# Optimization experiments

Measured on AMD Instinct MI355X. Metric: run time of the kernel, lower is better.

The kernel has to match this reference:

```python
import jax, jax.numpy as jnp
import numpy as np

B, T, S, O, D = 1024, 512, 8, 4, 64  # batch, seq_len, sensory_dim, output_dim, hidden d (d=64 from target_params=78980)


def _w(key, shape):
    # random weights scaled ~1/sqrt(fan_in); stored as [in, out] so y = x @ W + b
    return jax.random.normal(key, shape, dtype=jnp.float32) / np.sqrt(shape[0]).astype(np.float32)


def setup_inputs() -> dict:
    key = jax.random.key(0)
    ks = jax.random.split(key, 16)
    z = lambda n: jnp.zeros((n,), jnp.float32)
    return {
        "x": jax.random.normal(ks[0], (B, T, S), dtype=jnp.float32),
        "W_enc_w": _w(ks[1], (S, D)), "W_enc_b": z(D),
        "W_from_W": _w(ks[2], (D, D)), "W_from_I": _w(ks[3], (D, D)), "W_from_A": _w(ks[4], (D, D)),
        "W_gate_w": _w(ks[5], (2 * D, D)), "W_gate_b": z(D),
        "I_z_w": _w(ks[6], (3 * D, D)), "I_z_b": z(D),
        "I_r_w": _w(ks[7], (3 * D, D)), "I_r_b": z(D),
        "I_h_w": _w(ks[8], (3 * D, D)), "I_h_b": z(D),
        "A_from_W": _w(ks[9], (D, D)), "A_from_I": _w(ks[10], (D, D)), "A_from_A": _w(ks[11], (D, D)),
        "A_gate_w": _w(ks[12], (2 * D, D)), "A_gate_b": z(D),
        "phi_w": _w(ks[13], (D, O)), "phi_b": z(O),
    }


def reference(x, W_enc_w, W_enc_b, W_from_W, W_from_I, W_from_A, W_gate_w, W_gate_b,
              I_z_w, I_z_b, I_r_w, I_r_b, I_h_w, I_h_b,
              A_from_W, A_from_I, A_from_A, A_gate_w, A_gate_b, phi_w, phi_b):
    batch = x.shape[0]
    d = W_from_W.shape[0]

    def step(carry, x_t):
        W, I, A = carry  # each [B, d]
        xt = jnp.tanh(x_t @ W_enc_w + W_enc_b)
        W_in = xt + W @ W_from_W + I @ W_from_I + A @ W_from_A
        Wg = jax.nn.sigmoid(jnp.concatenate([I, A], -1) @ W_gate_w + W_gate_b)
        W_new = jnp.tanh(W_in) * Wg
        comb = jnp.concatenate([W_new, I, A], -1)  # [B, 3d]
        z = jax.nn.sigmoid(comb @ I_z_w + I_z_b)
        r = jax.nn.sigmoid(comb @ I_r_w + I_r_b)
        h = jnp.tanh(jnp.concatenate([W_new, r * I, A], -1) @ I_h_w + I_h_b)
        I_new = (1.0 - z) * I + z * h
        A_in = W_new @ A_from_W + I_new @ A_from_I + A @ A_from_A
        Ag = jax.nn.sigmoid(jnp.concatenate([W_new, I_new], -1) @ A_gate_w + A_gate_b)
        A_new = jnp.tanh(A_in) * Ag
        action = A_new @ phi_w + phi_b  # [B, O]
        return (W_new, I_new, A_new), action

    init = tuple(jnp.zeros((batch, d), x.dtype) for _ in range(3))
    _, actions = jax.lax.scan(step, init, jnp.swapaxes(x, 0, 1))  # [T, B, O]
    return jnp.swapaxes(actions, 0, 1)  # [B, T, O]
```

## Files before the change

### kernel.cpp

```cpp
#include <hip/hip_runtime.h>
#include <cstddef>
#include <cstdint>

#define T_LEN 512
#define O_DIM 4

typedef _Float16 f16x8 __attribute__((ext_vector_type(8)));
typedef float    f32x4 __attribute__((ext_vector_type(4)));

#define MFMA(a, b, c) __builtin_amdgcn_mfma_f32_16x16x32_f16((a), (b), (c), 0, 0, 0)

__device__ __forceinline__ float sigm_f(float x) {
    return __builtin_amdgcn_rcpf(1.0f + __builtin_amdgcn_exp2f(x * -1.44269504f));
}
__device__ __forceinline__ float tanh_f(float x) {
    float e = __builtin_amdgcn_exp2f(x * 2.88539008f);
    return __builtin_fmaf(-2.0f, __builtin_amdgcn_rcpf(e + 1.0f), 1.0f);
}

__device__ __forceinline__ f16x8 load_bt(const float* __restrict__ W, int k0, int n) {
    const int lane = threadIdx.x & 63;
    const float* p = W + (size_t)(k0 + ((lane >> 4) << 3)) * 64 + n;
    f16x8 r;
#pragma unroll
    for (int j = 0; j < 8; ++j) r[j] = (_Float16)p[(size_t)j * 64];
    return r;
}

__device__ __forceinline__ f16x8 ld_af(const _Float16* base, int kt) {
    const int lane = threadIdx.x & 63;
    const int m = lane & 15, q = lane >> 4;
    return *(const f16x8*)(base + m * 72 + kt * 32 + q * 8);
}

__global__ __launch_bounds__(256, 1) void ANIMAZeroExact_86887188398421_kernel(
    const float* __restrict__ x,
    const float* __restrict__ Wenc_w, const float* __restrict__ Wenc_b,
    const float* __restrict__ WfW, const float* __restrict__ WfI, const float* __restrict__ WfA,
    const float* __restrict__ Wg_w, const float* __restrict__ Wg_b,
    const float* __restrict__ Iz_w, const float* __restrict__ Iz_b,
    const float* __restrict__ Ir_w, const float* __restrict__ Ir_b,
    const float* __restrict__ Ih_w, const float* __restrict__ Ih_b,
    const float* __restrict__ AfW, const float* __restrict__ AfI, const float* __restrict__ AfA,
    const float* __restrict__ Ag_w, const float* __restrict__ Ag_b,
    const float* __restrict__ phi_w, const float* __restrict__ phi_b,
    float* __restrict__ out)
{
    __shared__ __align__(16) _Float16 Wl[16][72];
    __shared__ __align__(16) _Float16 Il[16][72];
    __shared__ __align__(16) _Float16 Al[16][72];
    __shared__ __align__(16) _Float16 Rl[16][72];
    __shared__ __align__(16) _Float16 Ahist[16][4][72];
    __shared__ __align__(16) float xbig[4][520];
    __shared__ __align__(16) float actb[4][64][4];

    const int tid  = threadIdx.x;
    const int w    = tid >> 6;
    const int lane = tid & 63;
    const int q    = lane >> 4;
    const int c    = lane & 15;
    const int n    = w * 16 + c;
    const int r0   = blockIdx.x * 4;

    for (int i = tid; i < 16 * 72; i += 256) {
        (&Wl[0][0])[i] = (_Float16)0.0f; (&Il[0][0])[i] = (_Float16)0.0f;
        (&Al[0][0])[i] = (_Float16)0.0f; (&Rl[0][0])[i] = (_Float16)0.0f;
    }

    f16x8 S1B[6], G1B[4], ZB[6], RB[6], HB[6], AB[6], AGB[4], phiB[2];
#pragma unroll
    for (int j = 0; j < 2; ++j) {
        S1B[j] = load_bt(WfW, 32 * j, n);  S1B[2 + j] = load_bt(WfI, 32 * j, n);  S1B[4 + j] = load_bt(WfA, 32 * j, n);
        AB[j]  = load_bt(AfW, 32 * j, n);  AB[2 + j]  = load_bt(AfI, 32 * j, n);  AB[4 + j]  = load_bt(AfA, 32 * j, n);
    }
#pragma unroll
    for (int j = 0; j < 4; ++j) { G1B[j] = load_bt(Wg_w, 32 * j, n); AGB[j] = load_bt(Ag_w, 32 * j, n); }
#pragma unroll
    for (int j = 0; j < 6; ++j) { ZB[j] = load_bt(Iz_w, 32 * j, n); RB[j] = load_bt(Ir_w, 32 * j, n); HB[j] = load_bt(Ih_w, 32 * j, n); }
#pragma unroll
    for (int kt = 0; kt < 2; ++kt)
#pragma unroll
        for (int j = 0; j < 8; ++j) {
            int k = kt * 32 + q * 8 + j;
            phiB[kt][j] = (c < O_DIM) ? (_Float16)phi_w[k * O_DIM + c] : (_Float16)0.0f;
        }

    float We[8];
#pragma unroll
    for (int j = 0; j < 8; ++j) We[j] = Wenc_w[j * 64 + n];

    const float bias_g  = Wg_b[n],  bias_z = Iz_b[n], bias_r = Ir_b[n];
    const float bias_h  = Ih_b[n],  bias_ag = Ag_b[n], bias_e = Wenc_b[n];
    const float bias_p  = (c < O_DIM) ? phi_b[c] : 0.0f;

    f32x4 zero4 = {0.f, 0.f, 0.f, 0.f};

    {
        const int prow = tid >> 6, psu = tid & 63;
        const float* xg = x + (size_t)(r0 + prow) * (T_LEN * 8) + (1 + psu) * 8;
        float4 pa = *(const float4*)(xg);
        float4 pb = *(const float4*)(xg + 4);
        float* d = &xbig[prow][psu * 8];
        *(float4*)d = pa; *(float4*)(d + 4) = pb;
    }
    float xt;
    {
        const float* xg = x + (size_t)(r0 + q) * (T_LEN * 8);
        float4 a = *(const float4*)(xg);
        float4 b = *(const float4*)(xg + 4);
        float d = bias_e;
        d = __builtin_fmaf(a.x, We[0], d); d = __builtin_fmaf(a.y, We[1], d);
        d = __builtin_fmaf(a.z, We[2], d); d = __builtin_fmaf(a.w, We[3], d);
        d = __builtin_fmaf(b.x, We[4], d); d = __builtin_fmaf(b.y, We[5], d);
        d = __builtin_fmaf(b.z, We[6], d); d = __builtin_fmaf(b.w, We[7], d);
        xt = tanh_f(d);
    }

    f32x4 w_a = zero4, w_b = zero4, g_a = zero4, g_b = zero4;
    f32x4 zp_a = zero4, zp_c = zero4, rp_a = zero4, rp_c = zero4;
    f32x4 hp_a, hp_c, ap_a, ap_c, ag_a, ag_c;
    float Iv = 0.f;
    f16x8 nW0, nW1;

    __syncthreads();

#pragma unroll 1
    for (int t = 0; t < T_LEN; ++t) {
        const bool fl16 = ((t & 15) == 0) && (t > 0);
        const bool fl64 = ((t & 63) == 0) && (t > 0);

        f16x8 sA0 = ld_af(&Al[0][0], 0), sA1 = ld_af(&Al[0][0], 1);
        float4 xra = {0,0,0,0}, xrb = {0,0,0,0};
        if (fl64) {
            const int rrow = tid >> 6, rsu = tid & 63;
            int off = (t + 1 + rsu) * 8;
            if (off > T_LEN * 8 - 8) off = T_LEN * 8 - 8;
            const float* xg = x + (size_t)(r0 + rrow) * (T_LEN * 8) + off;
            xra = *(const float4*)(xg); xrb = *(const float4*)(xg + 4);
        }
        w_a = MFMA(sA0, S1B[4], w_a);  w_b = MFMA(sA1, S1B[5], w_b);
        g_a = MFMA(sA0, G1B[2], g_a);  g_b = MFMA(sA1, G1B[3], g_b);
        {
            float wn = tanh_f(xt + w_a[0] + w_b[0]) * sigm_f(g_a[0] + g_b[0] + bias_g);
            Wl[4 * q][n] = (_Float16)wn;
        }
        zp_a = MFMA(sA0, ZB[4], zp_a);  zp_c = MFMA(sA1, ZB[5], zp_c);
        rp_a = MFMA(sA0, RB[4], rp_a);  rp_c = MFMA(sA1, RB[5], rp_c);
        __syncthreads();

        nW0 = ld_af(&Wl[0][0], 0); nW1 = ld_af(&Wl[0][0], 1);
        hp_a = MFMA(sA0, HB[4], zero4); hp_c = MFMA(sA1, HB[5], zero4);
        ap_a = MFMA(sA0, AB[4], zero4); ap_c = MFMA(sA1, AB[5], zero4);
        if (fl16) {
            const _Float16* ah = &Ahist[0][0][0];
            const int hw = (4 * w + (c >> 2)) * 288 + (c & 3) * 72 + 8 * q;
            f16x8 a0 = *(const f16x8*)(ah + hw);
            f16x8 a1 = *(const f16x8*)(ah + hw + 32);
            f32x4 act = MFMA(a0, phiB[0], zero4);
            act = MFMA(a1, phiB[1], act);
            if (c < O_DIM) {
                const int slot = (t - 16 + 4 * w + q) & 63;
#pragma unroll
                for (int rg = 0; rg < 4; ++rg)
                    actb[rg][slot][c] = act[rg] + bias_p;
            }
        }
        rp_a = MFMA(nW0, RB[0], rp_a);  rp_c = MFMA(nW1, RB[1], rp_c);
        {
            float rv = sigm_f(rp_a[0] + rp_c[0] + bias_r);
            Rl[4 * q][n] = (_Float16)(rv * Iv);
        }
        zp_a = MFMA(nW0, ZB[0], zp_a);  zp_c = MFMA(nW1, ZB[1], zp_c);
        hp_a = MFMA(nW0, HB[0], hp_a);  hp_c = MFMA(nW1, HB[1], hp_c);
        w_a  = MFMA(nW0, S1B[0], zero4); w_b = MFMA(nW1, S1B[1], zero4);
        if (fl64) {
            const int rrow = tid >> 6, rsu = tid & 63;
            float* d = &xbig[rrow][rsu * 8];
            *(float4*)d = xra; *(float4*)(d + 4) = xrb;
        }
        __syncthreads();

        f16x8 hR0 = ld_af(&Rl[0][0], 0), hR1 = ld_af(&Rl[0][0], 1);
        const float* xs = &xbig[q][(t & 63) * 8];
        float4 qa = *(const float4*)xs;
        float4 qb = *(const float4*)(xs + 4);
        ap_a = MFMA(nW0, AB[0], ap_a);  ap_c = MFMA(nW1, AB[1], ap_c);
        float zv = sigm_f(zp_a[0] + zp_c[0] + bias_z);
        float xtn;
        {
            float d = bias_e;
            d = __builtin_fmaf(qa.x, We[0], d); d = __builtin_fmaf(qa.y, We[1], d);
            d = __builtin_fmaf(qa.z, We[2], d); d = __builtin_fmaf(qa.w, We[3], d);
            d = __builtin_fmaf(qb.x, We[4], d); d = __builtin_fmaf(qb.y, We[5], d);
            d = __builtin_fmaf(qb.z, We[6], d); d = __builtin_fmaf(qb.w, We[7], d);
            xtn = tanh_f(d);
        }
        if (fl64) {
            const int frow = tid >> 6, fs = tid & 63;
            float4 av = *(const float4*)(&actb[frow][fs][0]);
            *(float4*)(out + (size_t)(r0 + frow) * (T_LEN * O_DIM) + (t - 64 + fs) * 4) = av;
        }
        hp_a = MFMA(hR0, HB[2], hp_a);  hp_c = MFMA(hR1, HB[3], hp_c);
        {
            float hv = tanh_f(hp_a[0] + hp_c[0] + bias_h);
            Iv = __builtin_fmaf(zv, hv - Iv, Iv);
            Il[4 * q][n] = (_Float16)Iv;
        }
        ag_a = MFMA(nW0, AGB[0], zero4); ag_c = MFMA(nW1, AGB[1], zero4);
        __syncthreads();

        f16x8 nI0 = ld_af(&Il[0][0], 0), nI1 = ld_af(&Il[0][0], 1);
        ap_a = MFMA(nI0, AB[2], ap_a);  ap_c = MFMA(nI1, AB[3], ap_c);
        ag_a = MFMA(nI0, AGB[2], ag_a); ag_c = MFMA(nI1, AGB[3], ag_c);
        {
            float av = tanh_f(ap_a[0] + ap_c[0]) * sigm_f(ag_a[0] + ag_c[0] + bias_ag);
            Al[4 * q][n] = (_Float16)av;
            Ahist[t & 15][q][n] = (_Float16)av;
        }
        w_a = MFMA(nI0, S1B[2], w_a);   w_b = MFMA(nI1, S1B[3], w_b);
        g_a = MFMA(nI0, G1B[0], zero4); g_b = MFMA(nI1, G1B[1], zero4);
        zp_a = MFMA(nI0, ZB[2], zero4); zp_c = MFMA(nI1, ZB[3], zero4);
        rp_a = MFMA(nI0, RB[2], zero4); rp_c = MFMA(nI1, RB[3], zero4);
        xt = xtn;
        __syncthreads();
    }

    {
        const _Float16* ah = &Ahist[0][0][0];
        const int hw = (4 * w + (c >> 2)) * 288 + (c & 3) * 72 + 8 * q;
        f16x8 a0 = *(const f16x8*)(ah + hw);
        f16x8 a1 = *(const f16x8*)(ah + hw + 32);
        f32x4 act = MFMA(a0, phiB[0], zero4);
        act = MFMA(a1, phiB[1], act);
        if (c < O_DIM) {
            const int slot = 48 + 4 * w + q;
#pragma unroll
            for (int rg = 0; rg < 4; ++rg)
                actb[rg][slot][c] = act[rg] + bias_p;
        }
        __syncthreads();
        const int frow = tid >> 6, fs = tid & 63;
        float4 av = *(const float4*)(&actb[frow][fs][0]);
        *(float4*)(out + (size_t)(r0 + frow) * (T_LEN * O_DIM) + (448 + fs) * 4) = av;
    }
}

extern "C" void kernel_launch(void* const* d_in, const int* in_sizes, int n_in,
                              void* d_out, int out_size, void* d_ws, size_t ws_size,
                              hipStream_t stream) {
    ANIMAZeroExact_86887188398421_kernel<<<dim3(256), dim3(256), 0, stream>>>(
        (const float*)d_in[0],
        (const float*)d_in[1],  (const float*)d_in[2],
        (const float*)d_in[3],  (const float*)d_in[4],  (const float*)d_in[5],
        (const float*)d_in[6],  (const float*)d_in[7],
        (const float*)d_in[8],  (const float*)d_in[9],
        (const float*)d_in[10], (const float*)d_in[11],
        (const float*)d_in[12], (const float*)d_in[13],
        (const float*)d_in[14], (const float*)d_in[15], (const float*)d_in[16],
        (const float*)d_in[17], (const float*)d_in[18],
        (const float*)d_in[19], (const float*)d_in[20],
        (float*)d_out);
}
```

Baseline: 458.5 us.

## Halve batch rows per block and run two blocks per CU

Each block now handles 2 batch rows instead of 4, so the grid doubles to 512 blocks, and the launch bounds ask for 2 blocks per CU. The x prefetch and output store indexing are remapped to the smaller tile. The intent is to hide the serial per-timestep latency of the recurrence (MFMA chains, transcendentals, barriers) by interleaving two independent blocks on each CU. The trade-off is that each 16-row MFMA tile now carries only 2 useful rows, so the total MFMA work wasted on padding doubles. Register and LDS pressure per CU also rise.

```diff
diff --git a/kernel.cpp b/kernel.cpp
--- a/kernel.cpp
+++ b/kernel.cpp
@@ -33,7 +33,7 @@
     return *(const f16x8*)(base + m * 72 + kt * 32 + q * 8);
 }
 
-__global__ __launch_bounds__(256, 1) void ANIMAZeroExact_86887188398421_kernel(
+__global__ __launch_bounds__(256, 2) void ANIMAZeroExact_86887188398421_kernel(
     const float* __restrict__ x,
     const float* __restrict__ Wenc_w, const float* __restrict__ Wenc_b,
     const float* __restrict__ WfW, const float* __restrict__ WfI, const float* __restrict__ WfA,
@@ -51,16 +51,24 @@
     __shared__ __align__(16) _Float16 Al[16][72];
     __shared__ __align__(16) _Float16 Rl[16][72];
     __shared__ __align__(16) _Float16 Ahist[16][4][72];
-    __shared__ __align__(16) float xbig[4][520];
-    __shared__ __align__(16) float actb[4][64][4];
+    __shared__ __align__(16) float xbig[2][520];
+    __shared__ __align__(16) float actb[2][64][4];
 
     const int tid  = threadIdx.x;
     const int w    = tid >> 6;
     const int lane = tid & 63;
     const int q    = lane >> 4;
+    const int qb   = q & 1;
     const int c    = lane & 15;
     const int n    = w * 16 + c;
-    const int r0   = blockIdx.x * 4;
+    const int r0   = blockIdx.x * 2;
+
+    const int prow = tid >> 7;
+    const int pidx = tid & 127;
+    const int psu  = pidx >> 1;
+    const int phl  = (pidx & 1) * 4;
+    const int frow = tid >> 6;
+    const int fs   = tid & 63;
 
     for (int i = tid; i < 16 * 72; i += 256) {
         (&Wl[0][0])[i] = (_Float16)0.0f; (&Il[0][0])[i] = (_Float16)0.0f;
@@ -96,16 +104,12 @@
     f32x4 zero4 = {0.f, 0.f, 0.f, 0.f};
 
     {
-        const int prow = tid >> 6, psu = tid & 63;
-        const float* xg = x + (size_t)(r0 + prow) * (T_LEN * 8) + (1 + psu) * 8;
-        float4 pa = *(const float4*)(xg);
-        float4 pb = *(const float4*)(xg + 4);
-        float* d = &xbig[prow][psu * 8];
-        *(float4*)d = pa; *(float4*)(d + 4) = pb;
+        const float* xg = x + (size_t)(r0 + prow) * (T_LEN * 8) + (1 + psu) * 8 + phl;
+        *(float4*)(&xbig[prow][psu * 8 + phl]) = *(const float4*)(xg);
     }
     float xt;
     {
-        const float* xg = x + (size_t)(r0 + q) * (T_LEN * 8);
+        const float* xg = x + (size_t)(r0 + qb) * (T_LEN * 8);
         float4 a = *(const float4*)(xg);
         float4 b = *(const float4*)(xg + 4);
         float d = bias_e;
@@ -130,13 +134,11 @@
         const bool fl64 = ((t & 63) == 0) && (t > 0);
 
         f16x8 sA0 = ld_af(&Al[0][0], 0), sA1 = ld_af(&Al[0][0], 1);
-        float4 xra = {0,0,0,0}, xrb = {0,0,0,0};
+        float4 xra = {0,0,0,0};
         if (fl64) {
-            const int rrow = tid >> 6, rsu = tid & 63;
-            int off = (t + 1 + rsu) * 8;
+            int off = (t + 1 + psu) * 8;
             if (off > T_LEN * 8 - 8) off = T_LEN * 8 - 8;
-            const float* xg = x + (size_t)(r0 + rrow) * (T_LEN * 8) + off;
-            xra = *(const float4*)(xg); xrb = *(const float4*)(xg + 4);
+            xra = *(const float4*)(x + (size_t)(r0 + prow) * (T_LEN * 8) + off + phl);
         }
         w_a = MFMA(sA0, S1B[4], w_a);  w_b = MFMA(sA1, S1B[5], w_b);
         g_a = MFMA(sA0, G1B[2], g_a);  g_b = MFMA(sA1, G1B[3], g_b);
@@ -161,7 +163,7 @@
             if (c < O_DIM) {
                 const int slot = (t - 16 + 4 * w + q) & 63;
 #pragma unroll
-                for (int rg = 0; rg < 4; ++rg)
+                for (int rg = 0; rg < 2; ++rg)
                     actb[rg][slot][c] = act[rg] + bias_p;
             }
         }
@@ -173,17 +175,14 @@
         zp_a = MFMA(nW0, ZB[0], zp_a);  zp_c = MFMA(nW1, ZB[1], zp_c);
         hp_a = MFMA(nW0, HB[0], hp_a);  hp_c = MFMA(nW1, HB[1], hp_c);
         w_a  = MFMA(nW0, S1B[0], zero4); w_b = MFMA(nW1, S1B[1], zero4);
-        if (fl64) {
-            const int rrow = tid >> 6, rsu = tid & 63;
-            float* d = &xbig[rrow][rsu * 8];
-            *(float4*)d = xra; *(float4*)(d + 4) = xrb;
-        }
+        if (fl64)
+            *(float4*)(&xbig[prow][psu * 8 + phl]) = xra;
         __syncthreads();
 
         f16x8 hR0 = ld_af(&Rl[0][0], 0), hR1 = ld_af(&Rl[0][0], 1);
-        const float* xs = &xbig[q][(t & 63) * 8];
+        const float* xs = &xbig[qb][(t & 63) * 8];
         float4 qa = *(const float4*)xs;
-        float4 qb = *(const float4*)(xs + 4);
+        float4 qb4 = *(const float4*)(xs + 4);
         ap_a = MFMA(nW0, AB[0], ap_a);  ap_c = MFMA(nW1, AB[1], ap_c);
         float zv = sigm_f(zp_a[0] + zp_c[0] + bias_z);
         float xtn;
@@ -191,12 +190,11 @@
             float d = bias_e;
             d = __builtin_fmaf(qa.x, We[0], d); d = __builtin_fmaf(qa.y, We[1], d);
             d = __builtin_fmaf(qa.z, We[2], d); d = __builtin_fmaf(qa.w, We[3], d);
-            d = __builtin_fmaf(qb.x, We[4], d); d = __builtin_fmaf(qb.y, We[5], d);
-            d = __builtin_fmaf(qb.z, We[6], d); d = __builtin_fmaf(qb.w, We[7], d);
+            d = __builtin_fmaf(qb4.x, We[4], d); d = __builtin_fmaf(qb4.y, We[5], d);
+            d = __builtin_fmaf(qb4.z, We[6], d); d = __builtin_fmaf(qb4.w, We[7], d);
             xtn = tanh_f(d);
         }
-        if (fl64) {
-            const int frow = tid >> 6, fs = tid & 63;
+        if (fl64 && tid < 128) {
             float4 av = *(const float4*)(&actb[frow][fs][0]);
             *(float4*)(out + (size_t)(r0 + frow) * (T_LEN * O_DIM) + (t - 64 + fs) * 4) = av;
         }
@@ -235,20 +233,21 @@
         if (c < O_DIM) {
             const int slot = 48 + 4 * w + q;
 #pragma unroll
-            for (int rg = 0; rg < 4; ++rg)
+            for (int rg = 0; rg < 2; ++rg)
                 actb[rg][slot][c] = act[rg] + bias_p;
         }
         __syncthreads();
-        const int frow = tid >> 6, fs = tid & 63;
-        float4 av = *(const float4*)(&actb[frow][fs][0]);
-        *(float4*)(out + (size_t)(r0 + frow) * (T_LEN * O_DIM) + (448 + fs) * 4) = av;
+        if (tid < 128) {
+            float4 av = *(const float4*)(&actb[frow][fs][0]);
+            *(float4*)(out + (size_t)(r0 + frow) * (T_LEN * O_DIM) + (448 + fs) * 4) = av;
+        }
     }
 }
 
 extern "C" void kernel_launch(void* const* d_in, const int* in_sizes, int n_in,
                               void* d_out, int out_size, void* d_ws, size_t ws_size,
                               hipStream_t stream) {
-    ANIMAZeroExact_86887188398421_kernel<<<dim3(256), dim3(256), 0, stream>>>(
+    ANIMAZeroExact_86887188398421_kernel<<<dim3(512), dim3(256), 0, stream>>>(
         (const float*)d_in[0],
         (const float*)d_in[1],  (const float*)d_in[2],
         (const float*)d_in[3],  (const float*)d_in[4],  (const float*)d_in[5],
```

Result: slower. 600.0 us (+30.9%).

## Split each block's rows into two interleaved independent recurrence streams

Applied to the files above, without the earlier changes.

Each block's four batch rows are split into two independent sub-batches, A and B, of two rows each. Each sub-batch has its own LDS state buffers, accumulators and activation history. The MFMA and gate computations of the two streams are interleaved within every timestep, so independent instructions can fill the latency gaps of the serial recurrence chain. The cost is twice as many MFMAs per step, each using only a small part of its 16-row tile, plus more registers and LDS.

```diff
diff --git a/kernel.cpp b/kernel.cpp
--- a/kernel.cpp
+++ b/kernel.cpp
@@ -46,11 +46,9 @@
     const float* __restrict__ phi_w, const float* __restrict__ phi_b,
     float* __restrict__ out)
 {
-    __shared__ __align__(16) _Float16 Wl[16][72];
-    __shared__ __align__(16) _Float16 Il[16][72];
-    __shared__ __align__(16) _Float16 Al[16][72];
-    __shared__ __align__(16) _Float16 Rl[16][72];
-    __shared__ __align__(16) _Float16 Ahist[16][4][72];
+    __shared__ __align__(16) _Float16 WlA[16][72], IlA[16][72], AlA[16][72], RlA[16][72];
+    __shared__ __align__(16) _Float16 WlB[16][72], IlB[16][72], AlB[16][72], RlB[16][72];
+    __shared__ __align__(16) _Float16 AhistA[16][4][72], AhistB[16][4][72];
     __shared__ __align__(16) float xbig[4][520];
     __shared__ __align__(16) float actb[4][64][4];
 
@@ -58,13 +56,21 @@
     const int w    = tid >> 6;
     const int lane = tid & 63;
     const int q    = lane >> 4;
+    const int qb   = q & 1;
     const int c    = lane & 15;
     const int n    = w * 16 + c;
     const int r0   = blockIdx.x * 4;
 
+    const int prow = tid >> 6;
+    const int psu  = tid & 63;
+    const int frow = tid >> 6;
+    const int fs   = tid & 63;
+
     for (int i = tid; i < 16 * 72; i += 256) {
-        (&Wl[0][0])[i] = (_Float16)0.0f; (&Il[0][0])[i] = (_Float16)0.0f;
-        (&Al[0][0])[i] = (_Float16)0.0f; (&Rl[0][0])[i] = (_Float16)0.0f;
+        (&WlA[0][0])[i] = (_Float16)0.0f; (&IlA[0][0])[i] = (_Float16)0.0f;
+        (&AlA[0][0])[i] = (_Float16)0.0f; (&RlA[0][0])[i] = (_Float16)0.0f;
+        (&WlB[0][0])[i] = (_Float16)0.0f; (&IlB[0][0])[i] = (_Float16)0.0f;
+        (&AlB[0][0])[i] = (_Float16)0.0f; (&RlB[0][0])[i] = (_Float16)0.0f;
     }
 
     f16x8 S1B[6], G1B[4], ZB[6], RB[6], HB[6], AB[6], AGB[4], phiB[2];
@@ -96,16 +102,15 @@
     f32x4 zero4 = {0.f, 0.f, 0.f, 0.f};
 
     {
-        const int prow = tid >> 6, psu = tid & 63;
         const float* xg = x + (size_t)(r0 + prow) * (T_LEN * 8) + (1 + psu) * 8;
-        float4 pa = *(const float4*)(xg);
-        float4 pb = *(const float4*)(xg + 4);
+        float4 a = *(const float4*)(xg);
+        float4 b = *(const float4*)(xg + 4);
         float* d = &xbig[prow][psu * 8];
-        *(float4*)d = pa; *(float4*)(d + 4) = pb;
-    }
-    float xt;
+        *(float4*)d = a; *(float4*)(d + 4) = b;
+    }
+    float xtA, xtB;
     {
-        const float* xg = x + (size_t)(r0 + q) * (T_LEN * 8);
+        const float* xg = x + (size_t)(r0 + qb) * (T_LEN * 8);
         float4 a = *(const float4*)(xg);
         float4 b = *(const float4*)(xg + 4);
         float d = bias_e;
@@ -113,14 +118,28 @@
         d = __builtin_fmaf(a.z, We[2], d); d = __builtin_fmaf(a.w, We[3], d);
         d = __builtin_fmaf(b.x, We[4], d); d = __builtin_fmaf(b.y, We[5], d);
         d = __builtin_fmaf(b.z, We[6], d); d = __builtin_fmaf(b.w, We[7], d);
-        xt = tanh_f(d);
-    }
-
-    f32x4 w_a = zero4, w_b = zero4, g_a = zero4, g_b = zero4;
-    f32x4 zp_a = zero4, zp_c = zero4, rp_a = zero4, rp_c = zero4;
-    f32x4 hp_a, hp_c, ap_a, ap_c, ag_a, ag_c;
-    float Iv = 0.f;
-    f16x8 nW0, nW1;
+        xtA = tanh_f(d);
+    }
+    {
+        const float* xg = x + (size_t)(r0 + 2 + qb) * (T_LEN * 8);
+        float4 a = *(const float4*)(xg);
+        float4 b = *(const float4*)(xg + 4);
+        float d = bias_e;
+        d = __builtin_fmaf(a.x, We[0], d); d = __builtin_fmaf(a.y, We[1], d);
+        d = __builtin_fmaf(a.z, We[2], d); d = __builtin_fmaf(a.w, We[3], d);
+        d = __builtin_fmaf(b.x, We[4], d); d = __builtin_fmaf(b.y, We[5], d);
+        d = __builtin_fmaf(b.z, We[6], d); d = __builtin_fmaf(b.w, We[7], d);
+        xtB = tanh_f(d);
+    }
+
+    f32x4 w_aA = zero4, w_bA = zero4, g_aA = zero4, g_bA = zero4;
+    f32x4 zp_aA = zero4, zp_cA = zero4, rp_aA = zero4, rp_cA = zero4;
+    f32x4 hp_aA, hp_cA, ap_aA, ap_cA, ag_aA, ag_cA;
+    f32x4 w_aB = zero4, w_bB = zero4, g_aB = zero4, g_bB = zero4;
+    f32x4 zp_aB = zero4, zp_cB = zero4, rp_aB = zero4, rp_cB = zero4;
+    f32x4 hp_aB, hp_cB, ap_aB, ap_cB, ag_aB, ag_cB;
+    float IvA = 0.f, IvB = 0.f;
+    f16x8 nW0A, nW1A, nW0B, nW1B;
 
     __syncthreads();
 
@@ -129,117 +148,194 @@
         const bool fl16 = ((t & 15) == 0) && (t > 0);
         const bool fl64 = ((t & 63) == 0) && (t > 0);
 
-        f16x8 sA0 = ld_af(&Al[0][0], 0), sA1 = ld_af(&Al[0][0], 1);
+        f16x8 sA0A = ld_af(&AlA[0][0], 0), sA1A = ld_af(&AlA[0][0], 1);
+        f16x8 sA0B = ld_af(&AlB[0][0], 0), sA1B = ld_af(&AlB[0][0], 1);
         float4 xra = {0,0,0,0}, xrb = {0,0,0,0};
         if (fl64) {
-            const int rrow = tid >> 6, rsu = tid & 63;
-            int off = (t + 1 + rsu) * 8;
+            int off = (t + 1 + psu) * 8;
             if (off > T_LEN * 8 - 8) off = T_LEN * 8 - 8;
-            const float* xg = x + (size_t)(r0 + rrow) * (T_LEN * 8) + off;
+            const float* xg = x + (size_t)(r0 + prow) * (T_LEN * 8) + off;
             xra = *(const float4*)(xg); xrb = *(const float4*)(xg + 4);
         }
-        w_a = MFMA(sA0, S1B[4], w_a);  w_b = MFMA(sA1, S1B[5], w_b);
-        g_a = MFMA(sA0, G1B[2], g_a);  g_b = MFMA(sA1, G1B[3], g_b);
-        {
-            float wn = tanh_f(xt + w_a[0] + w_b[0]) * sigm_f(g_a[0] + g_b[0] + bias_g);
-            Wl[4 * q][n] = (_Float16)wn;
-        }
-        zp_a = MFMA(sA0, ZB[4], zp_a);  zp_c = MFMA(sA1, ZB[5], zp_c);
-        rp_a = MFMA(sA0, RB[4], rp_a);  rp_c = MFMA(sA1, RB[5], rp_c);
-        __syncthreads();
-
-        nW0 = ld_af(&Wl[0][0], 0); nW1 = ld_af(&Wl[0][0], 1);
-        hp_a = MFMA(sA0, HB[4], zero4); hp_c = MFMA(sA1, HB[5], zero4);
-        ap_a = MFMA(sA0, AB[4], zero4); ap_c = MFMA(sA1, AB[5], zero4);
+        w_aA = MFMA(sA0A, S1B[4], w_aA);  w_bA = MFMA(sA1A, S1B[5], w_bA);
+        w_aB = MFMA(sA0B, S1B[4], w_aB);  w_bB = MFMA(sA1B, S1B[5], w_bB);
+        g_aA = MFMA(sA0A, G1B[2], g_aA);  g_bA = MFMA(sA1A, G1B[3], g_bA);
+        g_aB = MFMA(sA0B, G1B[2], g_aB);  g_bB = MFMA(sA1B, G1B[3], g_bB);
+        {
+            float wn = tanh_f(xtA + w_aA[0] + w_bA[0]) * sigm_f(g_aA[0] + g_bA[0] + bias_g);
+            WlA[4 * q][n] = (_Float16)wn;
+        }
+        {
+            float wn = tanh_f(xtB + w_aB[0] + w_bB[0]) * sigm_f(g_aB[0] + g_bB[0] + bias_g);
+            WlB[4 * q][n] = (_Float16)wn;
+        }
+        zp_aA = MFMA(sA0A, ZB[4], zp_aA);  zp_cA = MFMA(sA1A, ZB[5], zp_cA);
+        rp_aA = MFMA(sA0A, RB[4], rp_aA);  rp_cA = MFMA(sA1A, RB[5], rp_cA);
+        zp_aB = MFMA(sA0B, ZB[4], zp_aB);  zp_cB = MFMA(sA1B, ZB[5], zp_cB);
+        rp_aB = MFMA(sA0B, RB[4], rp_aB);  rp_cB = MFMA(sA1B, RB[5], rp_cB);
+        __syncthreads();
+
+        nW0A = ld_af(&WlA[0][0], 0); nW1A = ld_af(&WlA[0][0], 1);
+        nW0B = ld_af(&WlB[0][0], 0); nW1B = ld_af(&WlB[0][0], 1);
+        hp_aA = MFMA(sA0A, HB[4], zero4); hp_cA = MFMA(sA1A, HB[5], zero4);
+        hp_aB = MFMA(sA0B, HB[4], zero4); hp_cB = MFMA(sA1B, HB[5], zero4);
+        ap_aA = MFMA(sA0A, AB[4], zero4); ap_cA = MFMA(sA1A, AB[5], zero4);
+        ap_aB = MFMA(sA0B, AB[4], zero4); ap_cB = MFMA(sA1B, AB[5], zero4);
         if (fl16) {
-            const _Float16* ah = &Ahist[0][0][0];
             const int hw = (4 * w + (c >> 2)) * 288 + (c & 3) * 72 + 8 * q;
+            const int slot = (t - 16 + 4 * w + q) & 63;
+            {
+                const _Float16* ah = &AhistA[0][0][0];
+                f16x8 a0 = *(const f16x8*)(ah + hw);
+                f16x8 a1 = *(const f16x8*)(ah + hw + 32);
+                f32x4 act = MFMA(a0, phiB[0], zero4);
+                act = MFMA(a1, phiB[1], act);
+                if (c < O_DIM) {
+#pragma unroll
+                    for (int rg = 0; rg < 2; ++rg)
+                        actb[rg][slot][c] = act[rg] + bias_p;
+                }
+            }
+            {
+                const _Float16* ah = &AhistB[0][0][0];
+                f16x8 a0 = *(const f16x8*)(ah + hw);
+                f16x8 a1 = *(const f16x8*)(ah + hw + 32);
+                f32x4 act = MFMA(a0, phiB[0], zero4);
+                act = MFMA(a1, phiB[1], act);
+                if (c < O_DIM) {
+#pragma unroll
+                    for (int rg = 0; rg < 2; ++rg)
+                        actb[2 + rg][slot][c] = act[rg] + bias_p;
+                }
+            }
+        }
+        rp_aA = MFMA(nW0A, RB[0], rp_aA);  rp_cA = MFMA(nW1A, RB[1], rp_cA);
+        rp_aB = MFMA(nW0B, RB[0], rp_aB);  rp_cB = MFMA(nW1B, RB[1], rp_cB);
+        {
+            float rv = sigm_f(rp_aA[0] + rp_cA[0] + bias_r);
+            RlA[4 * q][n] = (_Float16)(rv * IvA);
+        }
+        {
+            float rv = sigm_f(rp_aB[0] + rp_cB[0] + bias_r);
+            RlB[4 * q][n] = (_Float16)(rv * IvB);
+        }
+        zp_aA = MFMA(nW0A, ZB[0], zp_aA);  zp_cA = MFMA(nW1A, ZB[1], zp_cA);
+        zp_aB = MFMA(nW0B, ZB[0], zp_aB);  zp_cB = MFMA(nW1B, ZB[1], zp_cB);
+        hp_aA = MFMA(nW0A, HB[0], hp_aA);  hp_cA = MFMA(nW1A, HB[1], hp_cA);
+        hp_aB = MFMA(nW0B, HB[0], hp_aB);  hp_cB = MFMA(nW1B, HB[1], hp_cB);
+        w_aA  = MFMA(nW0A, S1B[0], zero4); w_bA = MFMA(nW1A, S1B[1], zero4);
+        w_aB  = MFMA(nW0B, S1B[0], zero4); w_bB = MFMA(nW1B, S1B[1], zero4);
+        if (fl64) {
+            float* d = &xbig[prow][psu * 8];
+            *(float4*)d = xra; *(float4*)(d + 4) = xrb;
+        }
+        __syncthreads();
+
+        f16x8 hR0A = ld_af(&RlA[0][0], 0), hR1A = ld_af(&RlA[0][0], 1);
+        f16x8 hR0B = ld_af(&RlB[0][0], 0), hR1B = ld_af(&RlB[0][0], 1);
+        const float* xsA = &xbig[qb][(t & 63) * 8];
+        const float* xsB = &xbig[2 + qb][(t & 63) * 8];
+        float4 qaA = *(const float4*)xsA;
+        float4 qbA = *(const float4*)(xsA + 4);
+        float4 qaB = *(const float4*)xsB;
+        float4 qbB = *(const float4*)(xsB + 4);
+        ap_aA = MFMA(nW0A, AB[0], ap_aA);  ap_cA = MFMA(nW1A, AB[1], ap_cA);
+        ap_aB = MFMA(nW0B, AB[0], ap_aB);  ap_cB = MFMA(nW1B, AB[1], ap_cB);
+        float zvA = sigm_f(zp_aA[0] + zp_cA[0] + bias_z);
+        float zvB = sigm_f(zp_aB[0] + zp_cB[0] + bias_z);
+        float xtnA, xtnB;
+        {
+            float d = bias_e;
+            d = __builtin_fmaf(qaA.x, We[0], d); d = __builtin_fmaf(qaA.y, We[1], d);
+            d = __builtin_fmaf(qaA.z, We[2], d); d = __builtin_fmaf(qaA.w, We[3], d);
+            d = __builtin_fmaf(qbA.x, We[4], d); d = __builtin_fmaf(qbA.y, We[5], d);
+            d = __builtin_fmaf(qbA.z, We[6], d); d = __builtin_fmaf(qbA.w, We[7], d);
+            xtnA = tanh_f(d);
+        }
+        {
+            float d = bias_e;
+            d = __builtin_fmaf(qaB.x, We[0], d); d = __builtin_fmaf(qaB.y, We[1], d);
+            d = __builtin_fmaf(qaB.z, We[2], d); d = __builtin_fmaf(qaB.w, We[3], d);
+            d = __builtin_fmaf(qbB.x, We[4], d); d = __builtin_fmaf(qbB.y, We[5], d);
+            d = __builtin_fmaf(qbB.z, We[6], d); d = __builtin_fmaf(qbB.w, We[7], d);
+            xtnB = tanh_f(d);
+        }
+        if (fl64) {
+            float4 av = *(const float4*)(&actb[frow][fs][0]);
+            *(float4*)(out + (size_t)(r0 + frow) * (T_LEN * O_DIM) + (t - 64 + fs) * 4) = av;
+        }
+        hp_aA = MFMA(hR0A, HB[2], hp_aA);  hp_cA = MFMA(hR1A, HB[3], hp_cA);
+        hp_aB = MFMA(hR0B, HB[2], hp_aB);  hp_cB = MFMA(hR1B, HB[3], hp_cB);
+        {
+            float hv = tanh_f(hp_aA[0] + hp_cA[0] + bias_h);
+            IvA = __builtin_fmaf(zvA, hv - IvA, IvA);
+            IlA[4 * q][n] = (_Float16)IvA;
+        }
+        {
+            float hv = tanh_f(hp_aB[0] + hp_cB[0] + bias_h);
+            IvB = __builtin_fmaf(zvB, hv - IvB, IvB);
+            IlB[4 * q][n] = (_Float16)IvB;
+        }
+        ag_aA = MFMA(nW0A, AGB[0], zero4); ag_cA = MFMA(nW1A, AGB[1], zero4);
+        ag_aB = MFMA(nW0B, AGB[0], zero4); ag_cB = MFMA(nW1B, AGB[1], zero4);
+        __syncthreads();
+
+        f16x8 nI0A = ld_af(&IlA[0][0], 0), nI1A = ld_af(&IlA[0][0], 1);
+        f16x8 nI0B = ld_af(&IlB[0][0], 0), nI1B = ld_af(&IlB[0][0], 1);
+        ap_aA = MFMA(nI0A, AB[2], ap_aA);  ap_cA = MFMA(nI1A, AB[3], ap_cA);
+        ap_aB = MFMA(nI0B, AB[2], ap_aB);  ap_cB = MFMA(nI1B, AB[3], ap_cB);
+        ag_aA = MFMA(nI0A, AGB[2], ag_aA); ag_cA = MFMA(nI1A, AGB[3], ag_cA);
+        ag_aB = MFMA(nI0B, AGB[2], ag_aB); ag_cB = MFMA(nI1B, AGB[3], ag_cB);
+        {
+            float av = tanh_f(ap_aA[0] + ap_cA[0]) * sigm_f(ag_aA[0] + ag_cA[0] + bias_ag);
+            AlA[4 * q][n] = (_Float16)av;
+            AhistA[t & 15][q][n] = (_Float16)av;
+        }
+        {
+            float av = tanh_f(ap_aB[0] + ap_cB[0]) * sigm_f(ag_aB[0] + ag_cB[0] + bias_ag);
+            AlB[4 * q][n] = (_Float16)av;
+            AhistB[t & 15][q][n] = (_Float16)av;
+        }
+        w_aA = MFMA(nI0A, S1B[2], w_aA);   w_bA = MFMA(nI1A, S1B[3], w_bA);
+        w_aB = MFMA(nI0B, S1B[2], w_aB);   w_bB = MFMA(nI1B, S1B[3], w_bB);
+        g_aA = MFMA(nI0A, G1B[0], zero4);  g_bA = MFMA(nI1A, G1B[1], zero4);
+        g_aB = MFMA(nI0B, G1B[0], zero4);  g_bB = MFMA(nI1B, G1B[1], zero4);
+        zp_aA = MFMA(nI0A, ZB[2], zero4);  zp_cA = MFMA(nI1A, ZB[3], zero4);
+        zp_aB = MFMA(nI0B, ZB[2], zero4);  zp_cB = MFMA(nI1B, ZB[3], zero4);
+        rp_aA = MFMA(nI0A, RB[2], zero4);  rp_cA = MFMA(nI1A, RB[3], zero4);
+        rp_aB = MFMA(nI0B, RB[2], zero4);  rp_cB = MFMA(nI1B, RB[3], zero4);
+        xtA = xtnA; xtB = xtnB;
+        __syncthreads();
+    }
+
+    {
+        const int hw = (4 * w + (c >> 2)) * 288 + (c & 3) * 72 + 8 * q;
+        const int slot = 48 + 4 * w + q;
+        {
+            const _Float16* ah = &AhistA[0][0][0];
             f16x8 a0 = *(const f16x8*)(ah + hw);
             f16x8 a1 = *(const f16x8*)(ah + hw + 32);
             f32x4 act = MFMA(a0, phiB[0], zero4);
             act = MFMA(a1, phiB[1], act);
             if (c < O_DIM) {
-                const int slot = (t - 16 + 4 * w + q) & 63;
-#pragma unroll
-                for (int rg = 0; rg < 4; ++rg)
+#pragma unroll
+                for (int rg = 0; rg < 2; ++rg)
                     actb[rg][slot][c] = act[rg] + bias_p;
             }
         }
-        rp_a = MFMA(nW0, RB[0], rp_a);  rp_c = MFMA(nW1, RB[1], rp_c);
-        {
-            float rv = sigm_f(rp_a[0] + rp_c[0] + bias_r);
-            Rl[4 * q][n] = (_Float16)(rv * Iv);
-        }
-        zp_a = MFMA(nW0, ZB[0], zp_a);  zp_c = MFMA(nW1, ZB[1], zp_c);
-        hp_a = MFMA(nW0, HB[0], hp_a);  hp_c = MFMA(nW1, HB[1], hp_c);
-        w_a  = MFMA(nW0, S1B[0], zero4); w_b = MFMA(nW1, S1B[1], zero4);
-        if (fl64) {
-            const int rrow = tid >> 6, rsu = tid & 63;
-            float* d = &xbig[rrow][rsu * 8];
-            *(float4*)d = xra; *(float4*)(d + 4) = xrb;
-        }
-        __syncthreads();
-
-        f16x8 hR0 = ld_af(&Rl[0][0], 0), hR1 = ld_af(&Rl[0][0], 1);
-        const float* xs = &xbig[q][(t & 63) * 8];
-        float4 qa = *(const float4*)xs;
-        float4 qb = *(const float4*)(xs + 4);
-        ap_a = MFMA(nW0, AB[0], ap_a);  ap_c = MFMA(nW1, AB[1], ap_c);
-        float zv = sigm_f(zp_a[0] + zp_c[0] + bias_z);
-        float xtn;
-        {
-            float d = bias_e;
-            d = __builtin_fmaf(qa.x, We[0], d); d = __builtin_fmaf(qa.y, We[1], d);
-            d = __builtin_fmaf(qa.z, We[2], d); d = __builtin_fmaf(qa.w, We[3], d);
-            d = __builtin_fmaf(qb.x, We[4], d); d = __builtin_fmaf(qb.y, We[5], d);
-            d = __builtin_fmaf(qb.z, We[6], d); d = __builtin_fmaf(qb.w, We[7], d);
-            xtn = tanh_f(d);
-        }
-        if (fl64) {
-            const int frow = tid >> 6, fs = tid & 63;
-            float4 av = *(const float4*)(&actb[frow][fs][0]);
-            *(float4*)(out + (size_t)(r0 + frow) * (T_LEN * O_DIM) + (t - 64 + fs) * 4) = av;
-        }
-        hp_a = MFMA(hR0, HB[2], hp_a);  hp_c = MFMA(hR1, HB[3], hp_c);
-        {
-            float hv = tanh_f(hp_a[0] + hp_c[0] + bias_h);
-            Iv = __builtin_fmaf(zv, hv - Iv, Iv);
-            Il[4 * q][n] = (_Float16)Iv;
-        }
-        ag_a = MFMA(nW0, AGB[0], zero4); ag_c = MFMA(nW1, AGB[1], zero4);
-        __syncthreads();
-
-        f16x8 nI0 = ld_af(&Il[0][0], 0), nI1 = ld_af(&Il[0][0], 1);
-        ap_a = MFMA(nI0, AB[2], ap_a);  ap_c = MFMA(nI1, AB[3], ap_c);
-        ag_a = MFMA(nI0, AGB[2], ag_a); ag_c = MFMA(nI1, AGB[3], ag_c);
-        {
-            float av = tanh_f(ap_a[0] + ap_c[0]) * sigm_f(ag_a[0] + ag_c[0] + bias_ag);
-            Al[4 * q][n] = (_Float16)av;
-            Ahist[t & 15][q][n] = (_Float16)av;
-        }
-        w_a = MFMA(nI0, S1B[2], w_a);   w_b = MFMA(nI1, S1B[3], w_b);
-        g_a = MFMA(nI0, G1B[0], zero4); g_b = MFMA(nI1, G1B[1], zero4);
-        zp_a = MFMA(nI0, ZB[2], zero4); zp_c = MFMA(nI1, ZB[3], zero4);
-        rp_a = MFMA(nI0, RB[2], zero4); rp_c = MFMA(nI1, RB[3], zero4);
-        xt = xtn;
-        __syncthreads();
-    }
-
-    {
-        const _Float16* ah = &Ahist[0][0][0];
-        const int hw = (4 * w + (c >> 2)) * 288 + (c & 3) * 72 + 8 * q;
-        f16x8 a0 = *(const f16x8*)(ah + hw);
-        f16x8 a1 = *(const f16x8*)(ah + hw + 32);
-        f32x4 act = MFMA(a0, phiB[0], zero4);
-        act = MFMA(a1, phiB[1], act);
-        if (c < O_DIM) {
-            const int slot = 48 + 4 * w + q;
-#pragma unroll
-            for (int rg = 0; rg < 4; ++rg)
-                actb[rg][slot][c] = act[rg] + bias_p;
-        }
-        __syncthreads();
-        const int frow = tid >> 6, fs = tid & 63;
+        {
+            const _Float16* ah = &AhistB[0][0][0];
+            f16x8 a0 = *(const f16x8*)(ah + hw);
+            f16x8 a1 = *(const f16x8*)(ah + hw + 32);
+            f32x4 act = MFMA(a0, phiB[0], zero4);
+            act = MFMA(a1, phiB[1], act);
+            if (c < O_DIM) {
+#pragma unroll
+                for (int rg = 0; rg < 2; ++rg)
+                    actb[2 + rg][slot][c] = act[rg] + bias_p;
+            }
+        }
+        __syncthreads();
         float4 av = *(const float4*)(&actb[frow][fs][0]);
         *(float4*)(out + (size_t)(r0 + frow) * (T_LEN * O_DIM) + (448 + fs) * 4) = av;
     }
```

Result: slower. 710.8 us (+55.0%).
